# Kernel tuning notes

Hardware: AMD Instinct MI355X
Metric: run time of the kernel (lower is better)

Reference implementation:

```python
import jax, jax.numpy as jnp
import numpy as np

IMG_C = 256
GC = 32  # graph_channel; must equal graph feature dim 32 for the residual


def setup_inputs() -> dict:
    key = jax.random.key(0)
    ks = jax.random.split(key, 10)
    B, N, WH_SIDE = 8, 4096, 64
    s = lambda fan_in: 1.0 / np.sqrt(fan_in)
    return {
        "input_graph": jax.random.normal(ks[0], (B, N, GC), jnp.float32),
        "input_image": jax.random.normal(ks[1], (B, IMG_C, WH_SIDE, WH_SIDE), jnp.float32),
        # Conv1d(kernel=1) weights stored as [out, in]
        "Wq": jax.random.uniform(ks[2], (GC, 32), jnp.float32, -s(32), s(32)),
        "bq": jax.random.uniform(ks[3], (GC,), jnp.float32, -s(32), s(32)),
        "Wk": jax.random.uniform(ks[4], (GC, IMG_C), jnp.float32, -s(IMG_C), s(IMG_C)),
        "bk": jax.random.uniform(ks[5], (GC,), jnp.float32, -s(IMG_C), s(IMG_C)),
        "Wv": jax.random.uniform(ks[6], (GC, IMG_C), jnp.float32, -s(IMG_C), s(IMG_C)),
        "bv": jax.random.uniform(ks[7], (GC,), jnp.float32, -s(IMG_C), s(IMG_C)),
        "Wc": jax.random.uniform(ks[8], (GC, GC), jnp.float32, -s(GC), s(GC)),
        "bc": jax.random.uniform(ks[9], (GC,), jnp.float32, -s(GC), s(GC)),
    }


def reference(input_graph, input_image, Wq, bq, Wk, bk, Wv, bv, Wc, bc):
    B, C, W, H = input_image.shape
    img = input_image.reshape(B, C, W * H)                      # [B, C, L]
    # 1x1 conv projections == channel matmuls
    K = jnp.einsum('oc,bcl->bol', Wk, img) + bk[None, :, None]  # [B, GC, L]
    V = jnp.einsum('oc,bcl->bol', Wv, img) + bv[None, :, None]  # [B, GC, L]
    # Q: graph [B, N, 32] -> conv over channel dim -> [B, N, GC]
    Q = jnp.einsum('oc,bnc->bno', Wq, input_graph) + bq[None, None, :]
    att = jnp.einsum('bno,bol->bnl', Q, K) / jnp.sqrt(jnp.float32(GC))  # [B, N, L]
    # NOTE: original softmax is over dim=1 (the node/query axis)
    att = jax.nn.softmax(att, axis=1)
    message = jnp.einsum('bol,bnl->bon', V, att)                # [B, GC, N]
    out = input_graph.transpose(0, 2, 1) + (
        jnp.einsum('oc,bcn->bon', Wc, message) + bc[None, :, None]
    )                                                           # [B, GC, N]
    return out.transpose(0, 2, 1)                               # [B, N, GC]
```

## Files before the change

### kernel.cpp

```cpp
#include <hip/hip_runtime.h>

#define BB 8
#define NN 4096
#define LL 4096
#define CC 256

typedef short bf16x8 __attribute__((ext_vector_type(8)));
typedef _Float16 f16x8 __attribute__((ext_vector_type(8)));
typedef __fp16 hf16x2 __attribute__((ext_vector_type(2)));
typedef float f32x4 __attribute__((ext_vector_type(4)));

__device__ __forceinline__ short f2bf(float f) {
  union { float f; unsigned u; } v; v.f = f;
  unsigned r = v.u + 0x7fffu + ((v.u >> 16) & 1u);
  return (short)(r >> 16);
}
__device__ __forceinline__ bf16x8 ld8(const float* __restrict__ fp) {
  float4 a = *(const float4*)fp;
  float4 b = *(const float4*)(fp + 4);
  bf16x8 r;
  r[0] = f2bf(a.x); r[1] = f2bf(a.y); r[2] = f2bf(a.z); r[3] = f2bf(a.w);
  r[4] = f2bf(b.x); r[5] = f2bf(b.y); r[6] = f2bf(b.z); r[7] = f2bf(b.w);
  return r;
}

__global__ __launch_bounds__(256) void ka_proj(
    const float* __restrict__ graph, const float* __restrict__ img,
    const float* __restrict__ Wq, const float* __restrict__ bq,
    const float* __restrict__ Wk, const float* __restrict__ bk,
    const float* __restrict__ Wv, const float* __restrict__ bv,
    short* __restrict__ Qb, short* __restrict__ Kt, _Float16* __restrict__ Vt,
    float* __restrict__ Zbuf)
{
  const int tid = threadIdx.x;
  const int w = tid >> 6, lane = tid & 63, lo = lane & 15, q = lane >> 4;
  const int bid = blockIdx.x;
  if (bid < 512) {
    const int b = bid >> 6;
    if (tid < 64) Zbuf[(size_t)b * LL + ((bid & 63) << 6) + tid] = 0.0f;
    const int lt = ((bid & 63) << 6) + (w << 4);
    f32x4 aK0 = {0,0,0,0}, aK1 = {0,0,0,0}, aV0 = {0,0,0,0}, aV1 = {0,0,0,0};
    const float* ib = img + (size_t)b * CC * LL + lt + lo;
    #pragma unroll
    for (int cs = 0; cs < 8; ++cs) {
      const int c0 = cs * 32 + q * 8;
      bf16x8 bi;
      #pragma unroll
      for (int j = 0; j < 8; ++j) bi[j] = f2bf(ib[(size_t)(c0 + j) * LL]);
      bf16x8 wk0 = ld8(Wk + lo * CC + c0);
      bf16x8 wk1 = ld8(Wk + (lo + 16) * CC + c0);
      bf16x8 wv0 = ld8(Wv + lo * CC + c0);
      bf16x8 wv1 = ld8(Wv + (lo + 16) * CC + c0);
      aK0 = __builtin_amdgcn_mfma_f32_16x16x32_bf16(wk0, bi, aK0, 0, 0, 0);
      aK1 = __builtin_amdgcn_mfma_f32_16x16x32_bf16(wk1, bi, aK1, 0, 0, 0);
      aV0 = __builtin_amdgcn_mfma_f32_16x16x32_bf16(wv0, bi, aV0, 0, 0, 0);
      aV1 = __builtin_amdgcn_mfma_f32_16x16x32_bf16(wv1, bi, aV1, 0, 0, 0);
    }
    const float kscale = 0.2550348663f;
    const size_t row = ((size_t)b * LL + lt + lo) * 32;
    short4 s0, s1;
    s0.x = f2bf((aK0[0] + bk[q * 4 + 0]) * kscale);
    s0.y = f2bf((aK0[1] + bk[q * 4 + 1]) * kscale);
    s0.z = f2bf((aK0[2] + bk[q * 4 + 2]) * kscale);
    s0.w = f2bf((aK0[3] + bk[q * 4 + 3]) * kscale);
    s1.x = f2bf((aK1[0] + bk[16 + q * 4 + 0]) * kscale);
    s1.y = f2bf((aK1[1] + bk[16 + q * 4 + 1]) * kscale);
    s1.z = f2bf((aK1[2] + bk[16 + q * 4 + 2]) * kscale);
    s1.w = f2bf((aK1[3] + bk[16 + q * 4 + 3]) * kscale);
    *(short4*)(Kt + row + q * 4) = s0;
    *(short4*)(Kt + row + 16 + q * 4) = s1;
    union { hf16x2 h[2]; uint2 u; } p0, p1;
    p0.h[0] = __builtin_amdgcn_cvt_pkrtz(aV0[0] + bv[q * 4 + 0], aV0[1] + bv[q * 4 + 1]);
    p0.h[1] = __builtin_amdgcn_cvt_pkrtz(aV0[2] + bv[q * 4 + 2], aV0[3] + bv[q * 4 + 3]);
    p1.h[0] = __builtin_amdgcn_cvt_pkrtz(aV1[0] + bv[16 + q * 4 + 0], aV1[1] + bv[16 + q * 4 + 1]);
    p1.h[1] = __builtin_amdgcn_cvt_pkrtz(aV1[2] + bv[16 + q * 4 + 2], aV1[3] + bv[16 + q * 4 + 3]);
    *(uint2*)(Vt + row + q * 4) = p0.u;
    *(uint2*)(Vt + row + 16 + q * 4) = p1.u;
  } else {
    const int t = bid - 512;
    const int b = t >> 6;
    const int nt = ((t & 63) << 6) + (w << 4);
    bf16x8 ag = ld8(graph + ((size_t)b * NN + nt + lo) * 32 + q * 8);
    bf16x8 w0 = ld8(Wq + lo * 32 + q * 8);
    bf16x8 w1 = ld8(Wq + (lo + 16) * 32 + q * 8);
    f32x4 z = {0,0,0,0};
    f32x4 a0 = __builtin_amdgcn_mfma_f32_16x16x32_bf16(ag, w0, z, 0, 0, 0);
    f32x4 a1 = __builtin_amdgcn_mfma_f32_16x16x32_bf16(ag, w1, z, 0, 0, 0);
    const float b0 = bq[lo], b1 = bq[lo + 16];
    #pragma unroll
    for (int r = 0; r < 4; ++r) {
      const size_t rowq = ((size_t)b * NN + nt + q * 4 + r) * 32;
      Qb[rowq + lo] = f2bf(a0[r] + b0);
      Qb[rowq + 16 + lo] = f2bf(a1[r] + b1);
    }
  }
}

__global__ __launch_bounds__(256) void kb1_z(
    const short* __restrict__ Qb, const short* __restrict__ Kt,
    float* __restrict__ Z)
{
  const int tid = threadIdx.x;
  const int w = tid >> 6, lane = tid & 63, lo = lane & 15, q = lane >> 4;
  const int bid = blockIdx.x;
  const int b = bid & 7;
  const int t = bid >> 3;
  const int l0 = (t >> 2) << 7;
  const int nq = t & 3;
  bf16x8 kf[8];
  #pragma unroll
  for (int f = 0; f < 8; ++f)
    kf[f] = *(const bf16x8*)(Kt + ((size_t)b * LL + l0 + f * 16 + lo) * 32 + q * 8);
  float za[8][4] = {{0}};
  const short* qbase = Qb + ((size_t)b * NN + nq * 1024 + w * 256 + lo) * 32 + q * 8;
  #pragma unroll 4
  for (int it = 0; it < 16; ++it) {
    bf16x8 qf = *(const bf16x8*)(qbase + it * 512);
    #pragma unroll
    for (int f = 0; f < 8; ++f) {
      f32x4 z = {0,0,0,0};
      f32x4 c = __builtin_amdgcn_mfma_f32_16x16x32_bf16(kf[f], qf, z, 0, 0, 0);
      #pragma unroll
      for (int r = 0; r < 4; ++r) za[f][r] += __builtin_amdgcn_exp2f(c[r]);
    }
  }
  #pragma unroll
  for (int m = 1; m < 16; m <<= 1)
    #pragma unroll
    for (int f = 0; f < 8; ++f)
      #pragma unroll
      for (int r = 0; r < 4; ++r)
        za[f][r] += __shfl_xor(za[f][r], m, 64);
  if (lo == 0) {
    #pragma unroll
    for (int f = 0; f < 8; ++f)
      #pragma unroll
      for (int r = 0; r < 4; ++r)
        atomicAdd(&Z[(size_t)b * LL + l0 + f * 16 + q * 4 + r], za[f][r]);
  }
}

__global__ __launch_bounds__(256) void kb2_scale(
    const _Float16* __restrict__ Vt, const float* __restrict__ Z,
    _Float16* __restrict__ Vpp)
{
  const int tid = threadIdx.x;
  const int b = blockIdx.x >> 6;
  const int l = ((blockIdx.x & 63) << 6) + (tid & 63);
  const int og = tid >> 6;
  const float inv = __builtin_amdgcn_rcpf(Z[(size_t)b * LL + l]) * 4096.0f;
  const f16x8 vv = *(const f16x8*)(Vt + ((size_t)b * LL + l) * 32 + og * 8);
  #pragma unroll
  for (int j = 0; j < 8; ++j)
    Vpp[((size_t)b * 32 + og * 8 + j) * LL + l] = (_Float16)((float)vv[j] * inv);
}

__global__ __launch_bounds__(512) void kc_attn(
    const short* __restrict__ Qb, const short* __restrict__ Kt,
    const _Float16* __restrict__ Vpp, const float* __restrict__ graph,
    const float* __restrict__ Wc, const float* __restrict__ bc,
    float* __restrict__ out)
{
  __shared__ __align__(16) unsigned char smem[8 * 4608];
  const int tid = threadIdx.x;
  const int w = tid >> 6, lane = tid & 63, lo = lane & 15, q = lane >> 4;
  const int b = blockIdx.x & 7;
  const int n0 = ((int)blockIdx.x >> 3) << 7;
  _Float16* Pw = (_Float16*)(smem + w * 4608);
  bf16x8 qf[8];
  #pragma unroll
  for (int nq = 0; nq < 8; ++nq)
    qf[nq] = *(const bf16x8*)(Qb + ((size_t)b * NN + n0 + nq * 16 + lo) * 32 + q * 8);
  f32x4 m[8][2];
  #pragma unroll
  for (int nq = 0; nq < 8; ++nq) {
    m[nq][0] = (f32x4){0,0,0,0};
    m[nq][1] = (f32x4){0,0,0,0};
  }
  const short* ktb = Kt + (size_t)b * LL * 32 + lo * 32 + q * 8;
  const _Float16* vb0 = Vpp + ((size_t)b * 32 + lo) * LL;
  const _Float16* vb1 = vb0 + (size_t)16 * LL;
  const int lc0 = w * 8;
  for (int lc = lc0; lc < lc0 + 8; ++lc) {
    const int lbase = lc * 64;
    bf16x8 kf[4];
    #pragma unroll
    for (int f = 0; f < 4; ++f)
      kf[f] = *(const bf16x8*)(ktb + (size_t)(lbase + f * 16) * 32);
    f16x8 vA0 = *(const f16x8*)(vb0 + lbase + q * 8);
    f16x8 vA1 = *(const f16x8*)(vb0 + lbase + 32 + q * 8);
    f16x8 vB0 = *(const f16x8*)(vb1 + lbase + q * 8);
    f16x8 vB1 = *(const f16x8*)(vb1 + lbase + 32 + q * 8);
    #pragma unroll
    for (int p = 0; p < 4; ++p) {
      #pragma unroll
      for (int h = 0; h < 2; ++h) {
        const int nq = p * 2 + h;
        #pragma unroll
        for (int f = 0; f < 4; ++f) {
          f32x4 z = {0,0,0,0};
          f32x4 c = __builtin_amdgcn_mfma_f32_16x16x32_bf16(kf[f], qf[nq], z, 0, 0, 0);
          union { hf16x2 hh[2]; uint2 u; } pk;
          pk.hh[0] = __builtin_amdgcn_cvt_pkrtz(__builtin_amdgcn_exp2f(c[0]),
                                                __builtin_amdgcn_exp2f(c[1]));
          pk.hh[1] = __builtin_amdgcn_cvt_pkrtz(__builtin_amdgcn_exp2f(c[2]),
                                                __builtin_amdgcn_exp2f(c[3]));
          *(uint2*)&Pw[(h * 16 + lo) * 72 + f * 16 + q * 4] = pk.u;
        }
      }
      #pragma unroll
      for (int h = 0; h < 2; ++h) {
        const int nq = p * 2 + h;
        f16x8 pa0 = *(const f16x8*)&Pw[(h * 16 + lo) * 72 + q * 8];
        f16x8 pa1 = *(const f16x8*)&Pw[(h * 16 + lo) * 72 + 32 + q * 8];
        m[nq][0] = __builtin_amdgcn_mfma_f32_16x16x32_f16(pa0, vA0, m[nq][0], 0, 0, 0);
        m[nq][1] = __builtin_amdgcn_mfma_f32_16x16x32_f16(pa0, vB0, m[nq][1], 0, 0, 0);
        m[nq][0] = __builtin_amdgcn_mfma_f32_16x16x32_f16(pa1, vA1, m[nq][0], 0, 0, 0);
        m[nq][1] = __builtin_amdgcn_mfma_f32_16x16x32_f16(pa1, vB1, m[nq][1], 0, 0, 0);
      }
    }
  }
  const int o = lane & 31, nh = lane >> 5;
  float wcr[32];
  #pragma unroll
  for (int c4 = 0; c4 < 8; ++c4) {
    float4 wc4 = *(const float4*)(Wc + o * 32 + c4 * 4);
    wcr[c4 * 4 + 0] = wc4.x * (1.0f / 4096.0f);
    wcr[c4 * 4 + 1] = wc4.y * (1.0f / 4096.0f);
    wcr[c4 * 4 + 2] = wc4.z * (1.0f / 4096.0f);
    wcr[c4 * 4 + 3] = wc4.w * (1.0f / 4096.0f);
  }
  const float bcv = bc[o];
  float* MSw = (float*)(smem + w * 4608);
  const float* MS = (const float*)smem;
  #pragma unroll
  for (int p = 0; p < 4; ++p) {
    __syncthreads();
    #pragma unroll
    for (int h = 0; h < 2; ++h) {
      const int nq = p * 2 + h;
      #pragma unroll
      for (int r = 0; r < 4; ++r) {
        MSw[(h * 16 + q * 4 + r) * 36 + lo] = m[nq][0][r];
        MSw[(h * 16 + q * 4 + r) * 36 + 16 + lo] = m[nq][1][r];
      }
    }
    __syncthreads();
    #pragma unroll
    for (int rr = 0; rr < 2; ++rr) {
      const int nr = w * 4 + nh * 2 + rr;
      f32x4 s = {0,0,0,0};
      #pragma unroll
      for (int cc = 0; cc < 8; ++cc) {
        f32x4 a4 = *(const f32x4*)&MS[0 * 1152 + nr * 36 + cc * 4];
        #pragma unroll
        for (int k = 1; k < 8; ++k)
          a4 += *(const f32x4*)&MS[k * 1152 + nr * 36 + cc * 4];
        s[0] += wcr[cc * 4 + 0] * a4[0];
        s[1] += wcr[cc * 4 + 1] * a4[1];
        s[2] += wcr[cc * 4 + 2] * a4[2];
        s[3] += wcr[cc * 4 + 3] * a4[3];
      }
      const size_t idx = ((size_t)b * NN + n0 + p * 32 + nr) * 32 + o;
      out[idx] = s[0] + s[1] + s[2] + s[3] + bcv + graph[idx];
    }
  }
}

extern "C" void kernel_launch(void* const* d_in, const int* in_sizes, int n_in,
                              void* d_out, int out_size, void* d_ws, size_t ws_size,
                              hipStream_t stream) {
  const float* graph = (const float*)d_in[0];
  const float* img   = (const float*)d_in[1];
  const float* Wq    = (const float*)d_in[2];
  const float* bq    = (const float*)d_in[3];
  const float* Wk    = (const float*)d_in[4];
  const float* bk    = (const float*)d_in[5];
  const float* Wv    = (const float*)d_in[6];
  const float* bv    = (const float*)d_in[7];
  const float* Wc    = (const float*)d_in[8];
  const float* bc    = (const float*)d_in[9];
  char* ws = (char*)d_ws;
  short*    Qb  = (short*)(ws + 0);
  short*    Kt  = (short*)(ws + 2097152);
  _Float16* Vt  = (_Float16*)(ws + 4194304);
  _Float16* Vpp = (_Float16*)(ws + 6291456);
  float*    Zb  = (float*)(ws + 8388608);
  ka_proj<<<dim3(1024), dim3(256), 0, stream>>>(graph, img, Wq, bq, Wk, bk, Wv, bv,
                                                Qb, Kt, Vt, Zb);
  kb1_z<<<dim3(1024), dim3(256), 0, stream>>>(Qb, Kt, Zb);
  kb2_scale<<<dim3(512), dim3(256), 0, stream>>>(Vt, Zb, Vpp);
  kc_attn<<<dim3(256), dim3(512), 0, stream>>>(Qb, Kt, Vpp, graph, Wc, bc,
                                               (float*)d_out);
}
```

Baseline: 176.2 us.

## Fold softmax normalization into attention P tile and drop V rescale kernel

The projection kernel now writes V directly in channel-major layout, and the separate kernel that transposed and scaled V by 1/Z is replaced by a tiny kernel computing 4096/Z per column. The attention kernel multiplies each exp value by that inverse before packing to fp16, so V no longer needs an extra read/write pass. This removes a memory-bound kernel and its intermediate buffer, but adds per-element multiplies and extra float4 loads in the hot attention loop, and scattered 2-byte stores in the projection kernel.

Result: no change. 179.4 us (+1.8%).

```diff
diff --git a/kernel.cpp b/kernel.cpp
--- a/kernel.cpp
+++ b/kernel.cpp
@@ -29,7 +29,7 @@
     const float* __restrict__ Wq, const float* __restrict__ bq,
     const float* __restrict__ Wk, const float* __restrict__ bk,
     const float* __restrict__ Wv, const float* __restrict__ bv,
-    short* __restrict__ Qb, short* __restrict__ Kt, _Float16* __restrict__ Vt,
+    short* __restrict__ Qb, short* __restrict__ Kt, _Float16* __restrict__ Vt2,
     float* __restrict__ Zbuf)
 {
   const int tid = threadIdx.x;
@@ -69,13 +69,17 @@
     s1.w = f2bf((aK1[3] + bk[16 + q * 4 + 3]) * kscale);
     *(short4*)(Kt + row + q * 4) = s0;
     *(short4*)(Kt + row + 16 + q * 4) = s1;
-    union { hf16x2 h[2]; uint2 u; } p0, p1;
+    union { hf16x2 h[2]; __fp16 e[4]; } p0, p1;
     p0.h[0] = __builtin_amdgcn_cvt_pkrtz(aV0[0] + bv[q * 4 + 0], aV0[1] + bv[q * 4 + 1]);
     p0.h[1] = __builtin_amdgcn_cvt_pkrtz(aV0[2] + bv[q * 4 + 2], aV0[3] + bv[q * 4 + 3]);
     p1.h[0] = __builtin_amdgcn_cvt_pkrtz(aV1[0] + bv[16 + q * 4 + 0], aV1[1] + bv[16 + q * 4 + 1]);
     p1.h[1] = __builtin_amdgcn_cvt_pkrtz(aV1[2] + bv[16 + q * 4 + 2], aV1[3] + bv[16 + q * 4 + 3]);
-    *(uint2*)(Vt + row + q * 4) = p0.u;
-    *(uint2*)(Vt + row + 16 + q * 4) = p1.u;
+    const size_t vbase = (size_t)b * 32 * LL + lt + lo;
+    #pragma unroll
+    for (int r = 0; r < 4; ++r) {
+      Vt2[vbase + (size_t)(q * 4 + r) * LL] = p0.e[r];
+      Vt2[vbase + (size_t)(16 + q * 4 + r) * LL] = p1.e[r];
+    }
   } else {
     const int t = bid - 512;
     const int b = t >> 6;
@@ -140,26 +144,18 @@
   }
 }
 
-__global__ __launch_bounds__(256) void kb2_scale(
-    const _Float16* __restrict__ Vt, const float* __restrict__ Z,
-    _Float16* __restrict__ Vpp)
-{
-  const int tid = threadIdx.x;
-  const int b = blockIdx.x >> 6;
-  const int l = ((blockIdx.x & 63) << 6) + (tid & 63);
-  const int og = tid >> 6;
-  const float inv = __builtin_amdgcn_rcpf(Z[(size_t)b * LL + l]) * 4096.0f;
-  const f16x8 vv = *(const f16x8*)(Vt + ((size_t)b * LL + l) * 32 + og * 8);
-  #pragma unroll
-  for (int j = 0; j < 8; ++j)
-    Vpp[((size_t)b * 32 + og * 8 + j) * LL + l] = (_Float16)((float)vv[j] * inv);
+__global__ __launch_bounds__(256) void kz_inv(
+    const float* __restrict__ Z, float* __restrict__ Zi)
+{
+  const int i = blockIdx.x * 256 + threadIdx.x;
+  Zi[i] = 4096.0f * __builtin_amdgcn_rcpf(Z[i]);
 }
 
 __global__ __launch_bounds__(512) void kc_attn(
     const short* __restrict__ Qb, const short* __restrict__ Kt,
-    const _Float16* __restrict__ Vpp, const float* __restrict__ graph,
-    const float* __restrict__ Wc, const float* __restrict__ bc,
-    float* __restrict__ out)
+    const _Float16* __restrict__ Vt2, const float* __restrict__ Zi,
+    const float* __restrict__ graph, const float* __restrict__ Wc,
+    const float* __restrict__ bc, float* __restrict__ out)
 {
   __shared__ __align__(16) unsigned char smem[8 * 4608];
   const int tid = threadIdx.x;
@@ -178,11 +174,16 @@
     m[nq][1] = (f32x4){0,0,0,0};
   }
   const short* ktb = Kt + (size_t)b * LL * 32 + lo * 32 + q * 8;
-  const _Float16* vb0 = Vpp + ((size_t)b * 32 + lo) * LL;
+  const _Float16* vb0 = Vt2 + ((size_t)b * 32 + lo) * LL;
   const _Float16* vb1 = vb0 + (size_t)16 * LL;
+  const float* zib = Zi + b * 4096 + q * 4;
   const int lc0 = w * 8;
   for (int lc = lc0; lc < lc0 + 8; ++lc) {
     const int lbase = lc * 64;
+    float4 zi_[4];
+    #pragma unroll
+    for (int f = 0; f < 4; ++f)
+      zi_[f] = *(const float4*)(zib + lbase + f * 16);
     bf16x8 kf[4];
     #pragma unroll
     for (int f = 0; f < 4; ++f)
@@ -201,10 +202,12 @@
           f32x4 z = {0,0,0,0};
           f32x4 c = __builtin_amdgcn_mfma_f32_16x16x32_bf16(kf[f], qf[nq], z, 0, 0, 0);
           union { hf16x2 hh[2]; uint2 u; } pk;
-          pk.hh[0] = __builtin_amdgcn_cvt_pkrtz(__builtin_amdgcn_exp2f(c[0]),
-                                                __builtin_amdgcn_exp2f(c[1]));
-          pk.hh[1] = __builtin_amdgcn_cvt_pkrtz(__builtin_amdgcn_exp2f(c[2]),
-                                                __builtin_amdgcn_exp2f(c[3]));
+          pk.hh[0] = __builtin_amdgcn_cvt_pkrtz(
+              __builtin_amdgcn_exp2f(c[0]) * zi_[f].x,
+              __builtin_amdgcn_exp2f(c[1]) * zi_[f].y);
+          pk.hh[1] = __builtin_amdgcn_cvt_pkrtz(
+              __builtin_amdgcn_exp2f(c[2]) * zi_[f].z,
+              __builtin_amdgcn_exp2f(c[3]) * zi_[f].w);
           *(uint2*)&Pw[(h * 16 + lo) * 72 + f * 16 + q * 4] = pk.u;
         }
       }
@@ -283,13 +286,13 @@
   char* ws = (char*)d_ws;
   short*    Qb  = (short*)(ws + 0);
   short*    Kt  = (short*)(ws + 2097152);
-  _Float16* Vt  = (_Float16*)(ws + 4194304);
-  _Float16* Vpp = (_Float16*)(ws + 6291456);
-  float*    Zb  = (float*)(ws + 8388608);
+  _Float16* Vt2 = (_Float16*)(ws + 4194304);
+  float*    Zb  = (float*)(ws + 6291456);
+  float*    Zi  = (float*)(ws + 6422528);
   ka_proj<<<dim3(1024), dim3(256), 0, stream>>>(graph, img, Wq, bq, Wk, bk, Wv, bv,
-                                                Qb, Kt, Vt, Zb);
+                                                Qb, Kt, Vt2, Zb);
   kb1_z<<<dim3(1024), dim3(256), 0, stream>>>(Qb, Kt, Zb);
-  kb2_scale<<<dim3(512), dim3(256), 0, stream>>>(Vt, Zb, Vpp);
-  kc_attn<<<dim3(256), dim3(512), 0, stream>>>(Qb, Kt, Vpp, graph, Wc, bc,
+  kz_inv<<<dim3(128), dim3(256), 0, stream>>>(Zb, Zi);
+  kc_attn<<<dim3(256), dim3(512), 0, stream>>>(Qb, Kt, Vt2, Zi, graph, Wc, bc,
                                                (float*)d_out);
 }
```
